# Kernel optimization log

Measured on AMD Instinct MI355X. Metric: run time of the kernel, lower is better.

Reference implementation:

```python
import jax, jax.numpy as jnp
import numpy as np

B, S, H = 2, 2048, 2048
NH, NKV, HD = 32, 8, 64
MAXP = 4096


def _apply_rope(x, cos, sin, positions):
    # x: [b, h, s, d]; cos/sin: [max_pos, d//2]; positions: [b, s]
    c = cos[positions][:, None]  # [b,1,s,d/2]
    s_ = sin[positions][:, None]
    x1 = x[..., ::2]
    x2 = x[..., 1::2]
    rotated = jnp.stack((-x2, x1), axis=-1).reshape(x.shape)  # interleave
    c2 = jnp.concatenate([c, c], axis=-1)   # repeat(1,1,1,2) tiling
    s2 = jnp.concatenate([s_, s_], axis=-1)
    return x * c2 + rotated * s2


def setup_inputs() -> dict:
    key = jax.random.key(0)
    ks = jax.random.split(key, 10)
    hidden_states = jax.random.normal(ks[0], (B, S, H), dtype=jnp.float32)
    # RoPE tables (use real rotary tables for realism)
    inv_freq = 1.0 / (10000.0 ** (jnp.arange(0, HD, 2, dtype=jnp.float32) / HD))
    t = jnp.arange(MAXP, dtype=jnp.float32)
    freqs = jnp.outer(t, inv_freq)  # [max_pos, d/2]
    cos = jnp.cos(freqs)
    sin = jnp.sin(freqs)
    positions = jnp.broadcast_to(jnp.arange(S, dtype=jnp.int32), (B, S))
    # additive causal mask
    neg = jnp.finfo(jnp.float32).min
    mask = jnp.where(jnp.tril(jnp.ones((S, S), dtype=bool)), 0.0, neg)[None, None]
    sc = 1.0 / np.sqrt(H)
    q_w = jax.random.normal(ks[1], (NH * HD, H), dtype=jnp.float32) * sc
    q_b = jnp.zeros((NH * HD,), dtype=jnp.float32)
    k_w = jax.random.normal(ks[2], (NKV * HD, H), dtype=jnp.float32) * sc
    k_b = jnp.zeros((NKV * HD,), dtype=jnp.float32)
    v_w = jax.random.normal(ks[3], (NKV * HD, H), dtype=jnp.float32) * sc
    v_b = jnp.zeros((NKV * HD,), dtype=jnp.float32)
    o_w = jax.random.normal(ks[4], (H, NH * HD), dtype=jnp.float32) * sc
    return {"hidden_states": hidden_states, "cos": cos, "sin": sin,
            "positions": positions, "mask": mask,
            "q_w": q_w, "q_b": q_b, "k_w": k_w, "k_b": k_b,
            "v_w": v_w, "v_b": v_b, "o_w": o_w}


def reference(hidden_states, cos, sin, positions, mask, q_w, q_b, k_w, k_b, v_w, v_b, o_w):
    bsz, seq_len, _ = hidden_states.shape
    groups = NH // NKV
    q = (hidden_states @ q_w.T + q_b).reshape(bsz, seq_len, NH, HD).transpose(0, 2, 1, 3)
    k = (hidden_states @ k_w.T + k_b).reshape(bsz, seq_len, NKV, HD).transpose(0, 2, 1, 3)
    v = (hidden_states @ v_w.T + v_b).reshape(bsz, seq_len, NKV, HD).transpose(0, 2, 1, 3)
    q = _apply_rope(q, cos, sin, positions)
    k = _apply_rope(k, cos, sin, positions)
    if groups > 1:
        k = jnp.repeat(k, groups, axis=1)
        v = jnp.repeat(v, groups, axis=1)
    scale = 1.0 / np.sqrt(HD)
    attn = jnp.einsum('bhqd,bhkd->bhqk', q, k) * scale
    attn = attn + mask
    attn = jax.nn.softmax(attn.astype(jnp.float32), axis=-1).astype(q.dtype)
    out = jnp.einsum('bhqk,bhkd->bhqd', attn, v)
    out = out.transpose(0, 2, 1, 3).reshape(bsz, seq_len, NH * HD)
    return out @ o_w.T
```

## Files before the change

kernel.cpp:

```cpp
#include <hip/hip_runtime.h>
#include <hip/hip_bf16.h>

#define BB   2
#define SS   2048
#define HH   2048
#define NH   32
#define NKV  8
#define HD   64
#define NTOK (BB * SS)
#define NQKV (NH * HD + 2 * NKV * HD)
#define KOFF (NH * HD)
#define VOFF (NH * HD + NKV * HD)

#define QSC  0.1803368801111244f

typedef short  short8  __attribute__((ext_vector_type(8)));
typedef short  short4v __attribute__((ext_vector_type(4)));
typedef float  float4v __attribute__((ext_vector_type(4)));

using bf16 = __hip_bfloat16;

#define DEV static __device__ __forceinline__

DEV short8 load8(const bf16* p) { return *(const short8*)p; }
DEV short8 load8s(const short* p) { return *(const short8*)p; }

DEV short f2bfbits(float f) {
    union { bf16 h; short s; } u;
    u.h = __float2bfloat16(f);
    return u.s;
}

DEV unsigned int packbf2(float a, float b) {
    return (unsigned int)(unsigned short)f2bfbits(a)
         | ((unsigned int)(unsigned short)f2bfbits(b) << 16);
}

DEV void async16(const bf16* g, short* l) {
    __builtin_amdgcn_global_load_lds(
        (const __attribute__((address_space(1))) unsigned int*)g,
        (__attribute__((address_space(3))) unsigned int*)l, 16, 0, 0);
}

__global__ __launch_bounds__(256) void cvt_kernel(const float* __restrict__ src,
                                                  bf16* __restrict__ dst, int n) {
    int idx = (blockIdx.x * 256 + threadIdx.x) * 4;
    int stride = gridDim.x * 256 * 4;
    for (int i = idx; i < n; i += stride) {
        float4 v = *(const float4*)(src + i);
        short4v o;
        o[0] = f2bfbits(v.x); o[1] = f2bfbits(v.y);
        o[2] = f2bfbits(v.z); o[3] = f2bfbits(v.w);
        *(short4v*)(dst + i) = o;
    }
}

struct GemmCtx {
    const bf16 *gA0, *gA1, *gB0, *gB1;
    short *lA0, *lA1, *lB0, *lB1;
    const short *rdA, *rdB;
};

DEV void gemm_setup(GemmCtx& c, const bf16* A, const bf16* Bw, int K,
                    int m0, int n0, short* As, short* Bs) {
    int lane = threadIdx.x & 63, w = threadIdx.x >> 6;
    int quad = lane >> 4, tq = lane & 15;
    int srow = lane >> 2;
    int scol = (lane & 3) * 8;
    c.gA0 = A  + (size_t)(m0 + w * 32 + srow) * K + scol;
    c.gA1 = c.gA0 + (size_t)16 * K;
    c.gB0 = Bw + (size_t)(n0 + w * 32 + srow) * K + scol;
    c.gB1 = c.gB0 + (size_t)16 * K;
    c.lA0 = As + (w * 32) * 32;
    c.lA1 = As + (w * 32 + 16) * 32;
    c.lB0 = Bs + (w * 32) * 32;
    c.lB1 = Bs + (w * 32 + 16) * 32;
    int mbase = (w >> 1) * 64, nbase = (w & 1) * 64;
    c.rdA = As + (mbase + tq) * 32 + quad * 8;
    c.rdB = Bs + (nbase + tq) * 32 + quad * 8;
}

DEV void gemm_mainloop(GemmCtx& c, int K, float4v acc[4][4]) {
    for (int k0 = 0; k0 < K; k0 += 32) {
        __syncthreads();
        async16(c.gA0 + k0, c.lA0);
        async16(c.gA1 + k0, c.lA1);
        async16(c.gB0 + k0, c.lB0);
        async16(c.gB1 + k0, c.lB1);
        __syncthreads();
        short8 af[4], bfr[4];
#pragma unroll
        for (int mi = 0; mi < 4; ++mi) af[mi]  = *(const short8*)(c.rdA + mi * 16 * 32);
#pragma unroll
        for (int nj = 0; nj < 4; ++nj) bfr[nj] = *(const short8*)(c.rdB + nj * 16 * 32);
#pragma unroll
        for (int mi = 0; mi < 4; ++mi)
#pragma unroll
            for (int nj = 0; nj < 4; ++nj)
                acc[mi][nj] = __builtin_amdgcn_mfma_f32_16x16x32_bf16(
                    af[mi], bfr[nj], acc[mi][nj], 0, 0, 0);
    }
}

__global__ __launch_bounds__(256) void qkv_kernel(
    const bf16* __restrict__ Hb, const bf16* __restrict__ Wqkv,
    const float* __restrict__ qbias, const float* __restrict__ kbias,
    const float* __restrict__ vbias,
    const float* __restrict__ cosp, const float* __restrict__ sinp,
    const int* __restrict__ posp,
    bf16* __restrict__ Qb, bf16* __restrict__ Kb, bf16* __restrict__ Vt) {
    __shared__ __align__(16) short As[128 * 32];
    __shared__ __align__(16) short Bs[128 * 32];
    int lane = threadIdx.x & 63, w = threadIdx.x >> 6;
    int quad = lane >> 4, tq = lane & 15;
    int m0 = blockIdx.y * 128, n0 = blockIdx.x * 128;
    int mbase = (w >> 1) * 64, nbase = (w & 1) * 64;

    GemmCtx c;
    gemm_setup(c, Hb, Wqkv, HH, m0, n0, As, Bs);
    float4v acc[4][4] = {};
    gemm_mainloop(c, HH, acc);

    float biasv[4];
#pragma unroll
    for (int nj = 0; nj < 4; ++nj) {
        int colg = n0 + nbase + nj * 16 + tq;
        biasv[nj] = (colg < KOFF) ? qbias[colg]
                  : (colg < VOFF) ? kbias[colg - KOFF] : vbias[colg - VOFF];
    }

#pragma unroll
    for (int mi = 0; mi < 4; ++mi) {
#pragma unroll
        for (int r = 0; r < 4; ++r) {
            int tok = m0 + mbase + mi * 16 + quad * 4 + r;
            int p = posp[tok];
#pragma unroll
            for (int nj = 0; nj < 4; ++nj) {
                int colg = n0 + nbase + nj * 16 + tq;
                float val = acc[mi][nj][r] + biasv[nj];
                if (colg < VOFF) {
                    float pv = __shfl_xor(val, 1);
                    int jh = colg & 63;
                    float Cv = cosp[p * 32 + (jh & 31)];
                    float Sv = sinp[p * 32 + (jh & 31)];
                    float outv = (jh & 1) ? (val * Cv + pv * Sv)
                                          : (val * Cv - pv * Sv);
                    if (colg < KOFF)
                        Qb[(size_t)tok * (NH * HD) + colg] = __float2bfloat16(outv * QSC);
                    else
                        Kb[(size_t)tok * (NKV * HD) + (colg - KOFF)] = __float2bfloat16(outv);
                } else {
                    int c2 = colg - VOFF;
                    int kv = c2 >> 6, d = c2 & 63;
                    int bb = tok >> 11, s = tok & (SS - 1);
                    Vt[(((size_t)bb * NKV + kv) * HD + d) * SS + s] = __float2bfloat16(val);
                }
            }
        }
    }
}

__global__ __launch_bounds__(256) void oproj_kernel(
    const bf16* __restrict__ AO, const bf16* __restrict__ Wo,
    float* __restrict__ out) {
    __shared__ __align__(16) short As[128 * 32];
    __shared__ __align__(16) short Bs[128 * 32];
    int lane = threadIdx.x & 63, w = threadIdx.x >> 6;
    int quad = lane >> 4, tq = lane & 15;
    int m0 = blockIdx.y * 128, n0 = blockIdx.x * 128;
    int mbase = (w >> 1) * 64, nbase = (w & 1) * 64;

    GemmCtx c;
    gemm_setup(c, AO, Wo, NH * HD, m0, n0, As, Bs);
    float4v acc[4][4] = {};
    gemm_mainloop(c, NH * HD, acc);

#pragma unroll
    for (int mi = 0; mi < 4; ++mi) {
#pragma unroll
        for (int nj = 0; nj < 4; ++nj) {
            int colg = n0 + nbase + nj * 16 + tq;
#pragma unroll
            for (int r = 0; r < 4; ++r) {
                int tok = m0 + mbase + mi * 16 + quad * 4 + r;
                out[(size_t)tok * HH + colg] = acc[mi][nj][r];
            }
        }
    }
}

#define PST 72

template<bool MASK>
DEV void attn_kv_step(int kv0, int qw, int w, int lane, int quad, int tq,
                      const bf16* __restrict__ Kg, const bf16* __restrict__ Vg,
                      short* Ks, short* Vs, short* myp,
                      short8 aq0, short8 aq1,
                      float4v ot[4], float& lsum) {
    int srow = lane >> 3;
    int schunk = (lane & 7) ^ (srow & 7);

    __syncthreads();
#pragma unroll
    for (int cc = 0; cc < 2; ++cc) {
        int rl = w * 16 + cc * 8;
        async16(Kg + (size_t)(kv0 + rl + srow) * (NKV * HD) + schunk * 8,
                Ks + rl * 64);
        async16(Vg + (size_t)(rl + srow) * SS + kv0 + schunk * 8,
                Vs + rl * 64);
    }
    __syncthreads();

    int p0 = (quad ^ (tq & 7)) * 8;
    float4v st[4];
#pragma unroll
    for (int t = 0; t < 4; ++t) {
        const short* kr = Ks + (t * 16 + tq) * 64;
        short8 k0 = load8s(kr + p0);
        short8 k1 = load8s(kr + (p0 ^ 32));
        float4v s = {0.f, 0.f, 0.f, 0.f};
        s = __builtin_amdgcn_mfma_f32_16x16x32_bf16(k0, aq0, s, 0, 0, 0);
        s = __builtin_amdgcn_mfma_f32_16x16x32_bf16(k1, aq1, s, 0, 0, 0);
        st[t] = s;
    }

    short8 bv[4][2];
#pragma unroll
    for (int i = 0; i < 4; ++i) {
        const short* vr = Vs + (i * 16 + tq) * 64;
        bv[i][0] = load8s(vr + p0);
        bv[i][1] = load8s(vr + (p0 ^ 32));
    }

#pragma unroll
    for (int t = 0; t < 4; ++t) {
        float p[4];
#pragma unroll
        for (int r = 0; r < 4; ++r) {
            float e = __builtin_amdgcn_exp2f(st[t][r]);
            if (MASK) {
                int kvg = kv0 + t * 16 + quad * 4 + r;
                e = (kvg <= qw) ? e : 0.f;
            }
            p[r] = e;
            lsum += e;
        }
        int pos = tq * PST + t * 16 + quad * 4;
        *(unsigned int*)(myp + pos)     = packbf2(p[0], p[1]);
        *(unsigned int*)(myp + pos + 2) = packbf2(p[2], p[3]);
    }

    short8 pf0 = load8s(myp + tq * PST + quad * 8);
    short8 pf1 = load8s(myp + tq * PST + 32 + quad * 8);

#pragma unroll
    for (int i = 0; i < 4; ++i) {
        ot[i] = __builtin_amdgcn_mfma_f32_16x16x32_bf16(bv[i][0], pf0, ot[i], 0, 0, 0);
        ot[i] = __builtin_amdgcn_mfma_f32_16x16x32_bf16(bv[i][1], pf1, ot[i], 0, 0, 0);
    }
}

DEV void attn_qblock(int qb, int b, int h, int w, int lane, int quad, int tq,
                     const bf16* __restrict__ Qb,
                     const bf16* __restrict__ Kg, const bf16* __restrict__ Vg,
                     short* Ks, short* Vs, short* myp, bf16* __restrict__ AO) {
    int q0 = qb + w * 16;
    int qw = q0 + tq;
    const bf16* Qrow = Qb + (size_t)(b * SS + q0 + tq) * (NH * HD) + h * HD + quad * 8;
    short8 aq0 = load8(Qrow);
    short8 aq1 = load8(Qrow + 32);

    float4v ot[4] = {};
    float lsum = 0.f;

    for (int kv0 = 0; kv0 < qb; kv0 += 64)
        attn_kv_step<false>(kv0, qw, w, lane, quad, tq, Kg, Vg, Ks, Vs, myp,
                            aq0, aq1, ot, lsum);
    attn_kv_step<true>(qb, qw, w, lane, quad, tq, Kg, Vg, Ks, Vs, myp,
                       aq0, aq1, ot, lsum);

    lsum += __shfl_xor(lsum, 16);
    lsum += __shfl_xor(lsum, 32);
    float inv = 1.0f / lsum;

    bf16* obase = AO + (size_t)(b * SS + q0 + tq) * (NH * HD) + h * HD + quad * 4;
#pragma unroll
    for (int i = 0; i < 4; ++i) {
        short4v o;
#pragma unroll
        for (int r = 0; r < 4; ++r) o[r] = f2bfbits(ot[i][r] * inv);
        *(short4v*)(obase + i * 16) = o;
    }
}

__global__ __launch_bounds__(256, 4) void attn_kernel(
    const bf16* __restrict__ Qb, const bf16* __restrict__ Kb,
    const bf16* __restrict__ Vt, bf16* __restrict__ AO) {
    __shared__ __align__(16) short Ks[64 * 64];
    __shared__ __align__(16) short Vs[64 * 64];
    __shared__ __align__(16) short plds[4][16 * PST];

    int lane = threadIdx.x & 63, w = threadIdx.x >> 6;
    int quad = lane >> 4, tq = lane & 15;

    int x = blockIdx.x;
    int xcd = x & 7, xi = x >> 3;
    int pair = xcd * 2 + (xi & 1);
    int b = pair >> 3, kvh = pair & 7;
    int h = kvh * 4 + (xi >> 1);

    const bf16* Kg = Kb + (size_t)(b * SS) * (NKV * HD) + kvh * HD;
    const bf16* Vg = Vt + (size_t)((b * NKV + kvh) * HD) * SS;
    short* myp = &plds[w][0];

    int jq = blockIdx.y;
    attn_qblock((31 - jq) * 64, b, h, w, lane, quad, tq, Qb, Kg, Vg, Ks, Vs, myp, AO);
    attn_qblock(jq * 64,        b, h, w, lane, quad, tq, Qb, Kg, Vg, Ks, Vs, myp, AO);
}

extern "C" void kernel_launch(void* const* d_in, const int* in_sizes, int n_in,
                              void* d_out, int out_size, void* d_ws, size_t ws_size,
                              hipStream_t stream) {
    const float* hidden = (const float*)d_in[0];
    const float* cosp   = (const float*)d_in[1];
    const float* sinp   = (const float*)d_in[2];
    const int*   posp   = (const int*)d_in[3];
    const float* q_w = (const float*)d_in[5];
    const float* q_b = (const float*)d_in[6];
    const float* k_w = (const float*)d_in[7];
    const float* k_b = (const float*)d_in[8];
    const float* v_w = (const float*)d_in[9];
    const float* v_b = (const float*)d_in[10];
    const float* o_w = (const float*)d_in[11];
    float* out = (float*)d_out;

    char* ws = (char*)d_ws;
    bf16* Hb   = (bf16*)ws; ws += (size_t)NTOK * HH * 2;
    bf16* Wqkv = (bf16*)ws; ws += (size_t)NQKV * HH * 2;
    bf16* Wo   = (bf16*)ws; ws += (size_t)HH * (NH * HD) * 2;
    bf16* Qb   = (bf16*)ws; ws += (size_t)NTOK * (NH * HD) * 2;
    bf16* Kb   = (bf16*)ws; ws += (size_t)NTOK * (NKV * HD) * 2;
    bf16* Vt   = (bf16*)ws; ws += (size_t)NTOK * (NKV * HD) * 2;
    bf16* AO   = (bf16*)ws; ws += (size_t)NTOK * (NH * HD) * 2;

    cvt_kernel<<<2048, 256, 0, stream>>>(hidden, Hb, NTOK * HH);
    cvt_kernel<<<2048, 256, 0, stream>>>(q_w, Wqkv, (NH * HD) * HH);
    cvt_kernel<<<512, 256, 0, stream>>>(k_w, Wqkv + (size_t)KOFF * HH, (NKV * HD) * HH);
    cvt_kernel<<<512, 256, 0, stream>>>(v_w, Wqkv + (size_t)VOFF * HH, (NKV * HD) * HH);
    cvt_kernel<<<2048, 256, 0, stream>>>(o_w, Wo, HH * (NH * HD));

    qkv_kernel<<<dim3(NQKV / 128, NTOK / 128), 256, 0, stream>>>(
        Hb, Wqkv, q_b, k_b, v_b, cosp, sinp, posp, Qb, Kb, Vt);

    attn_kernel<<<dim3(64, 16), 256, 0, stream>>>(Qb, Kb, Vt, AO);

    oproj_kernel<<<dim3(HH / 128, NTOK / 128), 256, 0, stream>>>(AO, Wo, out);
}
```

Before: 334.3 us.

## Share K/V tile loads across paired query blocks and merge conversion launches

Result: slower. 464.6 us (+39.0%).

```diff
diff --git a/kernel.cpp b/kernel.cpp
--- a/kernel.cpp
+++ b/kernel.cpp
@@ -42,18 +42,28 @@
         (__attribute__((address_space(3))) unsigned int*)l, 16, 0, 0);
 }
 
-__global__ __launch_bounds__(256) void cvt_kernel(const float* __restrict__ src,
-                                                  bf16* __restrict__ dst, int n) {
-    int idx = (blockIdx.x * 256 + threadIdx.x) * 4;
-    int stride = gridDim.x * 256 * 4;
-    for (int i = idx; i < n; i += stride) {
-        float4 v = *(const float4*)(src + i);
-        short4v o;
-        o[0] = f2bfbits(v.x); o[1] = f2bfbits(v.y);
-        o[2] = f2bfbits(v.z); o[3] = f2bfbits(v.w);
-        *(short4v*)(dst + i) = o;
-    }
-}
+__global__ __launch_bounds__(256) void cvt_all_kernel(
+    const float* __restrict__ hidden, const float* __restrict__ q_w,
+    const float* __restrict__ k_w, const float* __restrict__ v_w,
+    const float* __restrict__ o_w,
+    bf16* __restrict__ Hb, bf16* __restrict__ Wqkv, bf16* __restrict__ Wo) {
+    int blk = blockIdx.x;
+    const float* src;
+    bf16* dst;
+    int off;
+    if (blk < 8192)       { src = hidden; dst = Hb;   off = blk * 1024; }
+    else if (blk < 12288) { src = q_w; dst = Wqkv;    off = (blk - 8192) * 1024; }
+    else if (blk < 13312) { src = k_w; dst = Wqkv + (size_t)KOFF * HH; off = (blk - 12288) * 1024; }
+    else if (blk < 14336) { src = v_w; dst = Wqkv + (size_t)VOFF * HH; off = (blk - 13312) * 1024; }
+    else                  { src = o_w; dst = Wo;      off = (blk - 14336) * 1024; }
+    int i = off + threadIdx.x * 4;
+    float4 v = *(const float4*)(src + i);
+    short4v o;
+    o[0] = f2bfbits(v.x); o[1] = f2bfbits(v.y);
+    o[2] = f2bfbits(v.z); o[3] = f2bfbits(v.w);
+    *(short4v*)(dst + i) = o;
+}
+#define CVT_BLOCKS 18432
 
 struct GemmCtx {
     const bf16 *gA0, *gA1, *gB0, *gB1;
@@ -192,27 +202,9 @@
 
 #define PST 72
 
-template<bool MASK>
-DEV void attn_kv_step(int kv0, int qw, int w, int lane, int quad, int tq,
-                      const bf16* __restrict__ Kg, const bf16* __restrict__ Vg,
-                      short* Ks, short* Vs, short* myp,
-                      short8 aq0, short8 aq1,
-                      float4v ot[4], float& lsum) {
-    int srow = lane >> 3;
-    int schunk = (lane & 7) ^ (srow & 7);
-
-    __syncthreads();
-#pragma unroll
-    for (int cc = 0; cc < 2; ++cc) {
-        int rl = w * 16 + cc * 8;
-        async16(Kg + (size_t)(kv0 + rl + srow) * (NKV * HD) + schunk * 8,
-                Ks + rl * 64);
-        async16(Vg + (size_t)(rl + srow) * SS + kv0 + schunk * 8,
-                Vs + rl * 64);
-    }
-    __syncthreads();
-
-    int p0 = (quad ^ (tq & 7)) * 8;
+DEV void attn_work(bool mask, int kv0, int qw, int quad, int tq, int p0,
+                   const short* Ks, const short* Vs, short* myp,
+                   short8 aq0, short8 aq1, float4v ot[4], float& lsum) {
     float4v st[4];
 #pragma unroll
     for (int t = 0; t < 4; ++t) {
@@ -225,21 +217,13 @@
         st[t] = s;
     }
 
-    short8 bv[4][2];
-#pragma unroll
-    for (int i = 0; i < 4; ++i) {
-        const short* vr = Vs + (i * 16 + tq) * 64;
-        bv[i][0] = load8s(vr + p0);
-        bv[i][1] = load8s(vr + (p0 ^ 32));
-    }
-
 #pragma unroll
     for (int t = 0; t < 4; ++t) {
         float p[4];
 #pragma unroll
         for (int r = 0; r < 4; ++r) {
             float e = __builtin_amdgcn_exp2f(st[t][r]);
-            if (MASK) {
+            if (mask) {
                 int kvg = kv0 + t * 16 + quad * 4 + r;
                 e = (kvg <= qw) ? e : 0.f;
             }
@@ -256,34 +240,19 @@
 
 #pragma unroll
     for (int i = 0; i < 4; ++i) {
-        ot[i] = __builtin_amdgcn_mfma_f32_16x16x32_bf16(bv[i][0], pf0, ot[i], 0, 0, 0);
-        ot[i] = __builtin_amdgcn_mfma_f32_16x16x32_bf16(bv[i][1], pf1, ot[i], 0, 0, 0);
-    }
-}
-
-DEV void attn_qblock(int qb, int b, int h, int w, int lane, int quad, int tq,
-                     const bf16* __restrict__ Qb,
-                     const bf16* __restrict__ Kg, const bf16* __restrict__ Vg,
-                     short* Ks, short* Vs, short* myp, bf16* __restrict__ AO) {
-    int q0 = qb + w * 16;
-    int qw = q0 + tq;
-    const bf16* Qrow = Qb + (size_t)(b * SS + q0 + tq) * (NH * HD) + h * HD + quad * 8;
-    short8 aq0 = load8(Qrow);
-    short8 aq1 = load8(Qrow + 32);
-
-    float4v ot[4] = {};
-    float lsum = 0.f;
-
-    for (int kv0 = 0; kv0 < qb; kv0 += 64)
-        attn_kv_step<false>(kv0, qw, w, lane, quad, tq, Kg, Vg, Ks, Vs, myp,
-                            aq0, aq1, ot, lsum);
-    attn_kv_step<true>(qb, qw, w, lane, quad, tq, Kg, Vg, Ks, Vs, myp,
-                       aq0, aq1, ot, lsum);
-
+        const short* vr = Vs + (i * 16 + tq) * 64;
+        short8 bv0 = load8s(vr + p0);
+        short8 bv1 = load8s(vr + (p0 ^ 32));
+        ot[i] = __builtin_amdgcn_mfma_f32_16x16x32_bf16(bv0, pf0, ot[i], 0, 0, 0);
+        ot[i] = __builtin_amdgcn_mfma_f32_16x16x32_bf16(bv1, pf1, ot[i], 0, 0, 0);
+    }
+}
+
+DEV void attn_epilogue(int q0, int b, int h, int quad, int tq,
+                       float4v ot[4], float lsum, bf16* __restrict__ AO) {
     lsum += __shfl_xor(lsum, 16);
     lsum += __shfl_xor(lsum, 32);
     float inv = 1.0f / lsum;
-
     bf16* obase = AO + (size_t)(b * SS + q0 + tq) * (NH * HD) + h * HD + quad * 4;
 #pragma unroll
     for (int i = 0; i < 4; ++i) {
@@ -315,8 +284,44 @@
     short* myp = &plds[w][0];
 
     int jq = blockIdx.y;
-    attn_qblock((31 - jq) * 64, b, h, w, lane, quad, tq, Qb, Kg, Vg, Ks, Vs, myp, AO);
-    attn_qblock(jq * 64,        b, h, w, lane, quad, tq, Qb, Kg, Vg, Ks, Vs, myp, AO);
+    int hi = (31 - jq) * 64, lo = jq * 64;
+
+    const bf16* Qh = Qb + (size_t)(b * SS + hi + w * 16 + tq) * (NH * HD) + h * HD + quad * 8;
+    const bf16* Ql = Qb + (size_t)(b * SS + lo + w * 16 + tq) * (NH * HD) + h * HD + quad * 8;
+    short8 aqh0 = load8(Qh), aqh1 = load8(Qh + 32);
+    short8 aql0 = load8(Ql), aql1 = load8(Ql + 32);
+
+    int qwh = hi + w * 16 + tq;
+    int qwl = lo + w * 16 + tq;
+
+    float4v oth[4] = {}, otl[4] = {};
+    float lsh = 0.f, lsl = 0.f;
+
+    int srow = lane >> 3;
+    int schunk = (lane & 7) ^ (srow & 7);
+    int p0 = (quad ^ (tq & 7)) * 8;
+
+    for (int kv0 = 0; kv0 <= hi; kv0 += 64) {
+        __syncthreads();
+#pragma unroll
+        for (int cc = 0; cc < 2; ++cc) {
+            int rl = w * 16 + cc * 8;
+            async16(Kg + (size_t)(kv0 + rl + srow) * (NKV * HD) + schunk * 8,
+                    Ks + rl * 64);
+            async16(Vg + (size_t)(rl + srow) * SS + kv0 + schunk * 8,
+                    Vs + rl * 64);
+        }
+        __syncthreads();
+
+        attn_work(kv0 == hi, kv0, qwh, quad, tq, p0, Ks, Vs, myp,
+                  aqh0, aqh1, oth, lsh);
+        if (kv0 <= lo)
+            attn_work(kv0 == lo, kv0, qwl, quad, tq, p0, Ks, Vs, myp,
+                      aql0, aql1, otl, lsl);
+    }
+
+    attn_epilogue(hi + w * 16, b, h, quad, tq, oth, lsh, AO);
+    attn_epilogue(lo + w * 16, b, h, quad, tq, otl, lsl, AO);
 }
 
 extern "C" void kernel_launch(void* const* d_in, const int* in_sizes, int n_in,
@@ -344,11 +349,8 @@
     bf16* Vt   = (bf16*)ws; ws += (size_t)NTOK * (NKV * HD) * 2;
     bf16* AO   = (bf16*)ws; ws += (size_t)NTOK * (NH * HD) * 2;
 
-    cvt_kernel<<<2048, 256, 0, stream>>>(hidden, Hb, NTOK * HH);
-    cvt_kernel<<<2048, 256, 0, stream>>>(q_w, Wqkv, (NH * HD) * HH);
-    cvt_kernel<<<512, 256, 0, stream>>>(k_w, Wqkv + (size_t)KOFF * HH, (NKV * HD) * HH);
-    cvt_kernel<<<512, 256, 0, stream>>>(v_w, Wqkv + (size_t)VOFF * HH, (NKV * HD) * HH);
-    cvt_kernel<<<2048, 256, 0, stream>>>(o_w, Wo, HH * (NH * HD));
+    cvt_all_kernel<<<CVT_BLOCKS, 256, 0, stream>>>(
+        hidden, q_w, k_w, v_w, o_w, Hb, Wqkv, Wo);
 
     qkv_kernel<<<dim3(NQKV / 128, NTOK / 128), 256, 0, stream>>>(
         Hb, Wqkv, q_b, k_b, v_b, cosp, sinp, posp, Qb, Kb, Vt);
```
